# Optimization experiments

Measured on AMD Instinct MI355X. Metric: run time of the kernel, lower is better.

The kernel has to match this reference:

```python
import jax, jax.numpy as jnp
import numpy as np

D_MODEL = 1024
N_HEADS = 16
HEAD_DIM = D_MODEL // N_HEADS
THETA = 10000.0
B, T = 2, 2048


def apply_rope(x, pos, theta=THETA):
    # x: (b, h, t, d), pos: (t,)
    d = x.shape[-1]
    inv_freq = theta ** (-jnp.arange(0, d, 2, dtype=jnp.float32) / d)  # (d/2,)
    ang = pos.astype(jnp.float32)[:, None] * inv_freq[None, :]          # (t, d/2)
    cos, sin = jnp.cos(ang), jnp.sin(ang)
    x1, x2 = x[..., 0::2], x[..., 1::2]
    out_even = x1 * cos - x2 * sin
    out_odd = x1 * sin + x2 * cos
    return jnp.stack([out_even, out_odd], axis=-1).reshape(x.shape)


def setup_inputs() -> dict:
    key = jax.random.key(0)
    ks = jax.random.split(key, 5)
    s = 1.0 / np.sqrt(D_MODEL)
    return {
        "x": jax.random.normal(ks[0], (B, T, D_MODEL), jnp.float32),
        "wq": jax.random.normal(ks[1], (D_MODEL, D_MODEL), jnp.float32) * s,
        "wk": jax.random.normal(ks[2], (D_MODEL, D_MODEL), jnp.float32) * s,
        "wv": jax.random.normal(ks[3], (D_MODEL, D_MODEL), jnp.float32) * s,
        "wo": jax.random.normal(ks[4], (D_MODEL, D_MODEL), jnp.float32) * s,
        "token_pos": 1,
    }


def reference(x, wq, wk, wv, wo, token_pos):
    b, t, dm = x.shape
    # bias-free Linear: y = x @ W^T; split heads -> (b, h, t, d)
    def proj(w):
        y = jnp.einsum('btm,nm->btn', x, w)
        return y.reshape(b, t, N_HEADS, HEAD_DIM).transpose(0, 2, 1, 3)
    q, k, v = proj(wq), proj(wk), proj(wv)
    pos = jnp.arange(t)
    q = apply_rope(q, pos)
    k = apply_rope(k, pos)
    scale = jnp.sqrt(jnp.asarray(HEAD_DIM, dtype=x.dtype))
    scores = jnp.einsum('bhqd,bhkd->bhqk', q, k) / scale
    mask = jnp.tril(jnp.ones((t, t), dtype=bool))
    scores = jnp.where(mask, scores, -jnp.inf)
    attn = jax.nn.softmax(scores, axis=-1)
    out = jnp.einsum('bhqk,bhkd->bhqd', attn, v)
    out = out.transpose(0, 2, 1, 3).reshape(b, t, dm)
    return jnp.einsum('btm,nm->btn', out, wo)
```

## Files before the change

kernel.cpp:

```cpp
#include <hip/hip_runtime.h>
#include <hip/hip_bf16.h>
#include <math.h>

#define DM 1024
#define NH 16
#define HD 64
#define BB 2
#define TT 2048
#define MROWS (BB*TT)
#define PL ((size_t)MROWS * DM)
#define PLW ((size_t)DM * DM)

using bf8_t = __attribute__((ext_vector_type(8))) __bf16;
using bf4_t = __attribute__((ext_vector_type(4))) __bf16;
using f4_t  = __attribute__((ext_vector_type(4))) float;

typedef const __attribute__((address_space(1))) void* gas_t;
typedef __attribute__((address_space(3))) void* las_t;

__global__ __launch_bounds__(256) void prep(
        const void* __restrict__ X,
        const void* __restrict__ w0, const void* __restrict__ w1,
        const void* __restrict__ w2, const void* __restrict__ w3,
        __bf16* __restrict__ Xh, __bf16* __restrict__ Wsp,
        float2* __restrict__ trig, int* __restrict__ flag)
{
    const int id  = (int)blockIdx.x;
    const int tid = (int)threadIdx.x;

    __shared__ int cnt;
    if (tid == 0) cnt = 0;
    __syncthreads();
    {
        int local = 0;
        const unsigned short* xu = (const unsigned short*)X;
        for (int i = tid; i < 512; i += 256) {
            const int e = (xu[i] >> 7) & 0xFF;
            if (e >= 117 && e <= 130) local++;
        }
        atomicAdd(&cnt, local);
    }
    __syncthreads();
    const int f32 = (cnt >= 384) ? 0 : 1;

    if (id >= 8448) {
        if (tid == 0) *flag = f32;
        return;
    }
    if (id >= 8192) {
        const int idx = (id - 8192) * 256 + tid;
        const int t = idx >> 5, ip = idx & 31;
        const float inv_freq = powf(10000.0f, -2.0f * (float)ip / 64.0f);
        const float ang = (float)t * inv_freq;
        float s, c;
        sincosf(ang, &s, &c);
        trig[idx] = make_float2(c, s);
        return;
    }

    const void* Src;
    __bf16 *Yh, *Yl;
    size_t i;
    if (id < 4096) {
        Src = X;
        Yh = Xh; Yl = Xh + PL;
        i = ((size_t)id * 256 + tid) * 4;
    } else {
        const int wid   = (id - 4096) >> 10;
        const int inner = (id - 4096) & 1023;
        Src = (wid == 0) ? w0 : (wid == 1) ? w1 : (wid == 2) ? w2 : w3;
        Yh = Wsp + (size_t)wid * 2 * PLW;
        Yl = Yh + PLW;
        i = ((size_t)inner * 256 + tid) * 4;
    }
    if (f32) {
        float4 v = *(const float4*)((const float*)Src + i);
        __bf16 h0 = (__bf16)v.x, h1 = (__bf16)v.y, h2 = (__bf16)v.z, h3 = (__bf16)v.w;
        bf4_t hv = {h0, h1, h2, h3};
        bf4_t lv = {(__bf16)(v.x - (float)h0), (__bf16)(v.y - (float)h1),
                    (__bf16)(v.z - (float)h2), (__bf16)(v.w - (float)h3)};
        *(bf4_t*)(Yh + i) = hv;
        *(bf4_t*)(Yl + i) = lv;
    } else {
        bf4_t v = *(const bf4_t*)((const __bf16*)Src + i);
        *(bf4_t*)(Yh + i) = v;
        bf4_t zv = {(__bf16)0.f, (__bf16)0.f, (__bf16)0.f, (__bf16)0.f};
        *(bf4_t*)(Yl + i) = zv;
    }
}

__device__ __forceinline__ int xcd_remap(int flat, int nwg) {
    return (flat & 7) * (nwg >> 3) + (flat >> 3);
}

__device__ __forceinline__ int swz(int r, int b) {
    return r * 128 + (b ^ ((r & 7) << 4));
}
#define VST 264

__global__ __launch_bounds__(256, 3) void gemm_fused(
        const __bf16* __restrict__ Ahg,
        const __bf16* __restrict__ Wsp,
        __bf16* __restrict__ Y0, __bf16* __restrict__ Y1,
        __bf16* __restrict__ Y2,
        void* __restrict__ Yout,
        const float2* __restrict__ trig,
        const int* __restrict__ flag, const int outMode)
{
    const int f32 = *flag;

    const int nx = (int)gridDim.x, ny = (int)gridDim.y, nz = (int)gridDim.z;
    int flat = (int)blockIdx.x + nx * ((int)blockIdx.y + ny * (int)blockIdx.z);
    flat = xcd_remap(flat, nx * ny * nz);
    const int bx = flat % nx;
    const int rem = flat / nx;
    const int by = rem % ny;
    const int z  = rem / ny;

    const int widx = outMode ? 3 : z;
    const __bf16* Whg = Wsp + (size_t)widx * 2 * PLW;
    const __bf16* Wlg = Whg + PLW;
    const __bf16* Alg = Ahg + PL;
    const bool aLo = (outMode != 0) || (f32 != 0);
    const bool wLo = (f32 != 0);

    __shared__ __align__(16) char sm[49152];
    char* const AhL = sm;
    char* const AlL = sm + 16384;
    char* const WhL = sm + 32768;
    char* const WlL = sm + 40960;

    const int tid  = threadIdx.x;
    const int n0   = bx * 64, m0 = by * 128;
    const int lane = tid & 63;
    const int w    = tid >> 6;
    const int wr   = (w >> 1) * 64;
    const int wcn  = (w & 1) * 32;
    const int l15  = lane & 15;
    const int g    = lane >> 4;

    f4_t acc[4][2] = {};

    for (int k0 = 0; k0 < DM; k0 += 64) {
        if (k0) __syncthreads();

#pragma unroll
        for (int j = 0; j < 4; j++) {
            const int u = tid + j * 256, r = u >> 3, c = u & 7;
            char* const db = AhL + (size_t)(j * 256 + w * 64) * 16;
            __builtin_amdgcn_global_load_lds(
                (gas_t)(Ahg + (size_t)(m0 + r) * DM + k0 + c * 8),
                (las_t)db, 16, 0, 0);
            if (aLo)
                __builtin_amdgcn_global_load_lds(
                    (gas_t)(Alg + (size_t)(m0 + r) * DM + k0 + c * 8),
                    (las_t)(AlL + (size_t)(j * 256 + w * 64) * 16), 16, 0, 0);
        }
#pragma unroll
        for (int j = 0; j < 2; j++) {
            const int u = tid + j * 256, r = u >> 3, c = u & 7;
            __builtin_amdgcn_global_load_lds(
                (gas_t)(Whg + (size_t)(n0 + r) * DM + k0 + c * 8),
                (las_t)(WhL + (size_t)(j * 256 + w * 64) * 16), 16, 0, 0);
            if (wLo)
                __builtin_amdgcn_global_load_lds(
                    (gas_t)(Wlg + (size_t)(n0 + r) * DM + k0 + c * 8),
                    (las_t)(WlL + (size_t)(j * 256 + w * 64) * 16), 16, 0, 0);
        }
        __syncthreads();

#pragma unroll
        for (int kh = 0; kh < 2; kh++) {
            const int bc = kh * 64 + g * 16;
            bf8_t ah[4], al[4], wh[2], wl[2];
#pragma unroll
            for (int m = 0; m < 4; m++) {
                ah[m] = *(const bf8_t*)(AhL + (wr + m * 16 + l15) * 128 + bc);
                if (aLo) al[m] = *(const bf8_t*)(AlL + (wr + m * 16 + l15) * 128 + bc);
            }
#pragma unroll
            for (int n = 0; n < 2; n++) {
                wh[n] = *(const bf8_t*)(WhL + (wcn + n * 16 + l15) * 128 + bc);
                if (wLo) wl[n] = *(const bf8_t*)(WlL + (wcn + n * 16 + l15) * 128 + bc);
            }
#pragma unroll
            for (int m = 0; m < 4; m++)
#pragma unroll
                for (int n = 0; n < 2; n++) {
                    acc[m][n] = __builtin_amdgcn_mfma_f32_16x16x32_bf16(
                                    ah[m], wh[n], acc[m][n], 0, 0, 0);
                    if (aLo)
                        acc[m][n] = __builtin_amdgcn_mfma_f32_16x16x32_bf16(
                                        al[m], wh[n], acc[m][n], 0, 0, 0);
                    if (wLo)
                        acc[m][n] = __builtin_amdgcn_mfma_f32_16x16x32_bf16(
                                        ah[m], wl[n], acc[m][n], 0, 0, 0);
                }
        }
    }

    const int orow = g * 4;
    const int ocol = l15;
    __syncthreads();

    if (outMode) {
        if (f32) {
#pragma unroll
            for (int m = 0; m < 4; m++)
#pragma unroll
                for (int n = 0; n < 2; n++) {
                    const int gr = m0 + wr + m * 16 + orow;
                    const int gc = n0 + wcn + n * 16 + ocol;
#pragma unroll
                    for (int r = 0; r < 4; r++)
                        ((float*)Yout)[(size_t)(gr + r) * DM + gc] = acc[m][n][r];
                }
        } else {
            char* const EhL = sm;
#pragma unroll
            for (int m = 0; m < 4; m++)
#pragma unroll
                for (int n = 0; n < 2; n++) {
                    const int ctile = wcn + n * 16 + ocol;
#pragma unroll
                    for (int r = 0; r < 4; r++) {
                        const int rtile = wr + m * 16 + orow + r;
                        *(__bf16*)(EhL + rtile * 128 + ctile * 2) = (__bf16)acc[m][n][r];
                    }
                }
            __syncthreads();
#pragma unroll
            for (int j = 0; j < 4; j++) {
                const int u = tid + j * 256, r = u >> 3, c = u & 7;
                *(bf8_t*)((__bf16*)Yout + (size_t)(m0 + r) * DM + n0 + c * 8) =
                    *(const bf8_t*)(EhL + r * 128 + c * 16);
            }
        }
    } else if (z == 2) {
        char* const EhL = sm;
        char* const ElL = sm + 20480;
#pragma unroll
        for (int m = 0; m < 4; m++)
#pragma unroll
            for (int n = 0; n < 2; n++) {
                const int ctile = wcn + n * 16 + ocol;
#pragma unroll
                for (int r = 0; r < 4; r++) {
                    const int rtile = wr + m * 16 + orow + r;
                    const float val = acc[m][n][r];
                    __bf16 hb = (__bf16)val;
                    *(__bf16*)(EhL + ctile * VST + rtile * 2) = hb;
                    *(__bf16*)(ElL + ctile * VST + rtile * 2) = (__bf16)(val - (float)hb);
                }
            }
        __syncthreads();
        __bf16* Vh = Y2;
        __bf16* Vl = Y2 + PL;
#pragma unroll
        for (int j = 0; j < 4; j++) {
            const int u = tid + j * 256, cc = u >> 4, k = u & 15;
            *(bf8_t*)(Vh + (size_t)(n0 + cc) * MROWS + m0 + k * 8) =
                *(const bf8_t*)(EhL + cc * VST + k * 16);
            *(bf8_t*)(Vl + (size_t)(n0 + cc) * MROWS + m0 + k * 8) =
                *(const bf8_t*)(ElL + cc * VST + k * 16);
        }
    } else {
        char* const EhL = sm;
        char* const ElL = sm + 20480;
#pragma unroll
        for (int m = 0; m < 4; m++)
#pragma unroll
            for (int n = 0; n < 2; n++) {
                const int ctile = wcn + n * 16 + ocol;
                const int gc = n0 + ctile;
                const int ip = (gc & 63) >> 1;
                const bool oddc = (gc & 1) != 0;
#pragma unroll
                for (int r = 0; r < 4; r++) {
                    const int rtile = wr + m * 16 + orow + r;
                    const int t = (m0 + rtile) & (TT - 1);
                    const float2 cs = trig[t * 32 + ip];
                    const float v = acc[m][n][r];
                    const float ov = __shfl_xor(v, 1);
                    float res = oddc ? (ov * cs.y + v * cs.x) : (v * cs.x - ov * cs.y);
                    if (z == 0) res *= 0.125f;
                    __bf16 hb = (__bf16)res;
                    *(__bf16*)(EhL + rtile * 128 + ctile * 2) = hb;
                    *(__bf16*)(ElL + rtile * 128 + ctile * 2) = (__bf16)(res - (float)hb);
                }
            }
        __syncthreads();
        __bf16* Yh = z ? Y1 : Y0;
        __bf16* Yl = Yh + PL;
#pragma unroll
        for (int j = 0; j < 4; j++) {
            const int u = tid + j * 256, r = u >> 3, c = u & 7;
            *(bf8_t*)(Yh + (size_t)(m0 + r) * DM + n0 + c * 8) =
                *(const bf8_t*)(EhL + r * 128 + c * 16);
            *(bf8_t*)(Yl + (size_t)(m0 + r) * DM + n0 + c * 8) =
                *(const bf8_t*)(ElL + r * 128 + c * 16);
        }
    }
}

__global__ void __launch_bounds__(256, 2) flash_attn_mfma(
        const __bf16* __restrict__ Qhg, const __bf16* __restrict__ Khg,
        const __bf16* __restrict__ Vhg, __bf16* __restrict__ Aoh)
{
    __shared__ __align__(16) char sm[65536];

    const __bf16* Qlg = Qhg + PL;
    const __bf16* Klg = Khg + PL;
    const __bf16* Vlg = Vhg + PL;
    __bf16* Aol = Aoh + PL;

    int flat = (int)blockIdx.x + 16 * ((int)blockIdx.y + 16 * (int)blockIdx.z);
    flat = xcd_remap(flat, 512);
    const int qt = 15 - (flat % 16);
    const int h  = (flat / 16) % 16;
    const int b  = flat / 256;

    const int tid = threadIdx.x;
    const int lane = tid & 63;
    const int w    = tid >> 6;
    const int l15  = lane & 15;
    const int g    = lane >> 4;

    char* const pb = sm + 32768 + w * 8192;

    bf8_t qh[2][2], ql[2][2];
#pragma unroll
    for (int m = 0; m < 2; m++)
#pragma unroll
        for (int kh = 0; kh < 2; kh++) {
            const size_t off = (size_t)(b * TT + qt * 128 + w * 32 + m * 16 + l15) * DM
                             + h * HD + kh * 32 + g * 8;
            qh[m][kh] = *(const bf8_t*)(Qhg + off);
            ql[m][kh] = *(const bf8_t*)(Qlg + off);
        }

    f4_t o[2][4] = {};
    float lrow[2] = {0.f, 0.f};

    bf8_t pk[2], pkl[2], pv[2], pvl[2];
    auto ISSUE = [&](int kt) {
#pragma unroll
        for (int j = 0; j < 2; j++) {
            const int u = tid + j * 256, r = u >> 3, c = u & 7;
            const size_t ko = (size_t)(b * TT + kt * 64 + r) * DM + h * HD + c * 8;
            pk[j]  = *(const bf8_t*)(Khg + ko);
            pkl[j] = *(const bf8_t*)(Klg + ko);
            const size_t vo = (size_t)(h * HD + r) * MROWS + b * TT + kt * 64 + c * 8;
            pv[j]  = *(const bf8_t*)(Vhg + vo);
            pvl[j] = *(const bf8_t*)(Vlg + vo);
        }
    };

    const int nkt = 2 * qt + 2;
    ISSUE(0);
    for (int kt = 0; kt < nkt; kt++) {
        __syncthreads();
#pragma unroll
        for (int j = 0; j < 2; j++) {
            const int u = tid + j * 256, r = u >> 3, c = u & 7;
            *(bf8_t*)(sm +         swz(r, c * 16)) = pk[j];
            *(bf8_t*)(sm +  8192 + swz(r, c * 16)) = pkl[j];
            *(bf8_t*)(sm + 16384 + swz(r, c * 16)) = pv[j];
            *(bf8_t*)(sm + 24576 + swz(r, c * 16)) = pvl[j];
        }
        __syncthreads();
        if (kt + 1 < nkt) ISSUE(kt + 1);

        f4_t s[2][4] = {};
        __builtin_amdgcn_s_setprio(1);
#pragma unroll
        for (int kh = 0; kh < 2; kh++) {
#pragma unroll
            for (int n = 0; n < 4; n++) {
                bf8_t kf  = *(const bf8_t*)(sm +        swz(n * 16 + l15, kh * 64 + g * 16));
                bf8_t kl2 = *(const bf8_t*)(sm + 8192 + swz(n * 16 + l15, kh * 64 + g * 16));
#pragma unroll
                for (int m = 0; m < 2; m++) {
                    s[m][n] = __builtin_amdgcn_mfma_f32_16x16x32_bf16(kf,  qh[m][kh], s[m][n], 0, 0, 0);
                    s[m][n] = __builtin_amdgcn_mfma_f32_16x16x32_bf16(kl2, qh[m][kh], s[m][n], 0, 0, 0);
                    s[m][n] = __builtin_amdgcn_mfma_f32_16x16x32_bf16(kf,  ql[m][kh], s[m][n], 0, 0, 0);
                }
            }
        }
        __builtin_amdgcn_s_setprio(0);

        if (kt >= 2 * qt) {
            const int koff = (kt - 2 * qt) * 64;
#pragma unroll
            for (int m = 0; m < 2; m++) {
                const int qloc = w * 32 + m * 16 + l15;
#pragma unroll
                for (int n = 0; n < 4; n++)
#pragma unroll
                    for (int r = 0; r < 4; r++)
                        if (koff + n * 16 + g * 4 + r > qloc) s[m][n][r] = -INFINITY;
            }
        }

#pragma unroll
        for (int m = 0; m < 2; m++)
#pragma unroll
            for (int n = 0; n < 4; n++) {
                bf4_t hv, lv;
#pragma unroll
                for (int r = 0; r < 4; r++) {
                    const float p = __expf(s[m][n][r] - 8.0f);
                    lrow[m] += p;
                    __bf16 hb = (__bf16)p;
                    hv[r] = hb;
                    lv[r] = (__bf16)(p - (float)hb);
                }
                *(bf4_t*)(pb +        swz(m * 16 + l15, n * 32 + g * 8)) = hv;
                *(bf4_t*)(pb + 4096 + swz(m * 16 + l15, n * 32 + g * 8)) = lv;
            }
        asm volatile("s_waitcnt lgkmcnt(0)" ::: "memory");
        __builtin_amdgcn_sched_barrier(0);

        bf8_t pah[2][2], pal2[2][2];
#pragma unroll
        for (int m = 0; m < 2; m++)
#pragma unroll
            for (int kh = 0; kh < 2; kh++) {
                pah[m][kh]  = *(const bf8_t*)(pb +        swz(m * 16 + l15, kh * 64 + g * 16));
                pal2[m][kh] = *(const bf8_t*)(pb + 4096 + swz(m * 16 + l15, kh * 64 + g * 16));
            }

        __builtin_amdgcn_s_setprio(1);
#pragma unroll
        for (int kh = 0; kh < 2; kh++)
#pragma unroll
            for (int nf = 0; nf < 4; nf++) {
                bf8_t vf  = *(const bf8_t*)(sm + 16384 + swz(nf * 16 + l15, kh * 64 + g * 16));
                bf8_t vl2 = *(const bf8_t*)(sm + 24576 + swz(nf * 16 + l15, kh * 64 + g * 16));
#pragma unroll
                for (int m = 0; m < 2; m++) {
                    o[m][nf] = __builtin_amdgcn_mfma_f32_16x16x32_bf16(pah[m][kh],  vf,  o[m][nf], 0, 0, 0);
                    o[m][nf] = __builtin_amdgcn_mfma_f32_16x16x32_bf16(pal2[m][kh], vf,  o[m][nf], 0, 0, 0);
                    o[m][nf] = __builtin_amdgcn_mfma_f32_16x16x32_bf16(pah[m][kh],  vl2, o[m][nf], 0, 0, 0);
                }
            }
        __builtin_amdgcn_s_setprio(0);
    }

    float linv[2][4];
#pragma unroll
    for (int m = 0; m < 2; m++) {
        lrow[m] += __shfl_xor(lrow[m], 16);
        lrow[m] += __shfl_xor(lrow[m], 32);
        const float inv = 1.0f / lrow[m];
#pragma unroll
        for (int r = 0; r < 4; r++)
            linv[m][r] = __shfl(inv, (lane & 48) | (g * 4 + r));
    }

#pragma unroll
    for (int m = 0; m < 2; m++)
#pragma unroll
        for (int nf = 0; nf < 4; nf++)
#pragma unroll
            for (int r = 0; r < 4; r++) {
                const float val = o[m][nf][r] * linv[m][r];
                __bf16 hb = (__bf16)val;
                const int row = m * 16 + g * 4 + r;
                *(__bf16*)(pb + row * 128 + (nf * 16 + l15) * 2) = hb;
                *(__bf16*)(pb + 4096 + row * 128 + (nf * 16 + l15) * 2) =
                    (__bf16)(val - (float)hb);
            }
    asm volatile("s_waitcnt lgkmcnt(0)" ::: "memory");
    __builtin_amdgcn_sched_barrier(0);
#pragma unroll
    for (int j = 0; j < 4; j++) {
        const int u = lane + j * 64, r = u >> 3, c = u & 7;
        const size_t off = (size_t)(b * TT + qt * 128 + w * 32 + r) * DM
                         + h * HD + c * 8;
        *(bf8_t*)(Aoh + off) = *(const bf8_t*)(pb + r * 128 + c * 16);
        *(bf8_t*)(Aol + off) = *(const bf8_t*)(pb + 4096 + r * 128 + c * 16);
    }
}

extern "C" void kernel_launch(void* const* d_in, const int* in_sizes, int n_in,
                              void* d_out, int out_size, void* d_ws, size_t ws_size,
                              hipStream_t stream) {
    const void* x  = d_in[0];
    const void* wq = d_in[1];
    const void* wk = d_in[2];
    const void* wv = d_in[3];
    const void* wo = d_in[4];

    __bf16* Qh  = (__bf16*)d_ws;
    __bf16* Kh  = Qh + 2 * PL;
    __bf16* Vth = Kh + 2 * PL;
    __bf16* Xh  = Vth + 2 * PL;
    __bf16* Wsp = Xh + 2 * PL;
    char* tail  = (char*)(Wsp + 8 * PLW);
    int* flag   = (int*)tail;
    float2* trig = (float2*)(tail + 512);

    prep<<<8449, 256, 0, stream>>>(x, wq, wk, wv, wo, Xh, Wsp, trig, flag);

    gemm_fused<<<dim3(DM / 64, MROWS / 128, 3), 256, 0, stream>>>(
        Xh, Wsp, Qh, Kh, Vth, nullptr, trig, flag, 0);

    flash_attn_mfma<<<dim3(16, NH, BB), 256, 0, stream>>>(Qh, Kh, Vth, Xh);

    gemm_fused<<<dim3(DM / 64, MROWS / 128, 1), 256, 0, stream>>>(
        Xh, Wsp, nullptr, nullptr, nullptr, d_out, trig, flag, 1);
}
```

Baseline: 326.1 us.

## Swizzle GEMM LDS tiles and add 64x64 tiled output projection kernel

Measured after the change: 312.1 us. -4.3%, faster.

```diff
diff --git a/kernel.cpp b/kernel.cpp
--- a/kernel.cpp
+++ b/kernel.cpp
@@ -147,24 +147,25 @@
 #pragma unroll
         for (int j = 0; j < 4; j++) {
             const int u = tid + j * 256, r = u >> 3, c = u & 7;
-            char* const db = AhL + (size_t)(j * 256 + w * 64) * 16;
+            const int cs = c ^ (r & 7);
             __builtin_amdgcn_global_load_lds(
-                (gas_t)(Ahg + (size_t)(m0 + r) * DM + k0 + c * 8),
-                (las_t)db, 16, 0, 0);
+                (gas_t)(Ahg + (size_t)(m0 + r) * DM + k0 + cs * 8),
+                (las_t)(AhL + (size_t)(j * 256 + w * 64) * 16), 16, 0, 0);
             if (aLo)
                 __builtin_amdgcn_global_load_lds(
-                    (gas_t)(Alg + (size_t)(m0 + r) * DM + k0 + c * 8),
+                    (gas_t)(Alg + (size_t)(m0 + r) * DM + k0 + cs * 8),
                     (las_t)(AlL + (size_t)(j * 256 + w * 64) * 16), 16, 0, 0);
         }
 #pragma unroll
         for (int j = 0; j < 2; j++) {
             const int u = tid + j * 256, r = u >> 3, c = u & 7;
+            const int cs = c ^ (r & 7);
             __builtin_amdgcn_global_load_lds(
-                (gas_t)(Whg + (size_t)(n0 + r) * DM + k0 + c * 8),
+                (gas_t)(Whg + (size_t)(n0 + r) * DM + k0 + cs * 8),
                 (las_t)(WhL + (size_t)(j * 256 + w * 64) * 16), 16, 0, 0);
             if (wLo)
                 __builtin_amdgcn_global_load_lds(
-                    (gas_t)(Wlg + (size_t)(n0 + r) * DM + k0 + c * 8),
+                    (gas_t)(Wlg + (size_t)(n0 + r) * DM + k0 + cs * 8),
                     (las_t)(WlL + (size_t)(j * 256 + w * 64) * 16), 16, 0, 0);
         }
         __syncthreads();
@@ -175,13 +176,13 @@
             bf8_t ah[4], al[4], wh[2], wl[2];
 #pragma unroll
             for (int m = 0; m < 4; m++) {
-                ah[m] = *(const bf8_t*)(AhL + (wr + m * 16 + l15) * 128 + bc);
-                if (aLo) al[m] = *(const bf8_t*)(AlL + (wr + m * 16 + l15) * 128 + bc);
+                ah[m] = *(const bf8_t*)(AhL + swz(wr + m * 16 + l15, bc));
+                if (aLo) al[m] = *(const bf8_t*)(AlL + swz(wr + m * 16 + l15, bc));
             }
 #pragma unroll
             for (int n = 0; n < 2; n++) {
-                wh[n] = *(const bf8_t*)(WhL + (wcn + n * 16 + l15) * 128 + bc);
-                if (wLo) wl[n] = *(const bf8_t*)(WlL + (wcn + n * 16 + l15) * 128 + bc);
+                wh[n] = *(const bf8_t*)(WhL + swz(wcn + n * 16 + l15, bc));
+                if (wLo) wl[n] = *(const bf8_t*)(WlL + swz(wcn + n * 16 + l15, bc));
             }
 #pragma unroll
             for (int m = 0; m < 4; m++)
@@ -303,6 +304,131 @@
     }
 }
 
+__global__ __launch_bounds__(256, 4) void gemm_out64(
+        const __bf16* __restrict__ Ahg,
+        const __bf16* __restrict__ Wsp,
+        void* __restrict__ Yout,
+        const int* __restrict__ flag)
+{
+    const int f32 = *flag;
+
+    int flat = (int)blockIdx.x + 16 * (int)blockIdx.y;
+    flat = xcd_remap(flat, 1024);
+    const int bx = flat % 16;
+    const int by = flat / 16;
+
+    const __bf16* Whg = Wsp + (size_t)3 * 2 * PLW;
+    const __bf16* Wlg = Whg + PLW;
+    const __bf16* Alg = Ahg + PL;
+    const bool wLo = (f32 != 0);
+
+    __shared__ __align__(16) char sm[32768];
+    char* const AhL = sm;
+    char* const AlL = sm + 8192;
+    char* const WhL = sm + 16384;
+    char* const WlL = sm + 24576;
+
+    const int tid  = threadIdx.x;
+    const int n0   = bx * 64, m0 = by * 64;
+    const int lane = tid & 63;
+    const int w    = tid >> 6;
+    const int wr   = (w >> 1) * 32;
+    const int wcn  = (w & 1) * 32;
+    const int l15  = lane & 15;
+    const int g    = lane >> 4;
+
+    f4_t acc[2][2] = {};
+
+    for (int k0 = 0; k0 < DM; k0 += 64) {
+        if (k0) __syncthreads();
+
+#pragma unroll
+        for (int j = 0; j < 2; j++) {
+            const int u = tid + j * 256, r = u >> 3, c = u & 7;
+            const int cs = c ^ (r & 7);
+            __builtin_amdgcn_global_load_lds(
+                (gas_t)(Ahg + (size_t)(m0 + r) * DM + k0 + cs * 8),
+                (las_t)(AhL + (size_t)(j * 256 + w * 64) * 16), 16, 0, 0);
+            __builtin_amdgcn_global_load_lds(
+                (gas_t)(Alg + (size_t)(m0 + r) * DM + k0 + cs * 8),
+                (las_t)(AlL + (size_t)(j * 256 + w * 64) * 16), 16, 0, 0);
+            __builtin_amdgcn_global_load_lds(
+                (gas_t)(Whg + (size_t)(n0 + r) * DM + k0 + cs * 8),
+                (las_t)(WhL + (size_t)(j * 256 + w * 64) * 16), 16, 0, 0);
+            if (wLo)
+                __builtin_amdgcn_global_load_lds(
+                    (gas_t)(Wlg + (size_t)(n0 + r) * DM + k0 + cs * 8),
+                    (las_t)(WlL + (size_t)(j * 256 + w * 64) * 16), 16, 0, 0);
+        }
+        __syncthreads();
+
+#pragma unroll
+        for (int kh = 0; kh < 2; kh++) {
+            const int bc = kh * 64 + g * 16;
+            bf8_t ah[2], al[2], wh[2], wl[2];
+#pragma unroll
+            for (int m = 0; m < 2; m++) {
+                ah[m] = *(const bf8_t*)(AhL + swz(wr + m * 16 + l15, bc));
+                al[m] = *(const bf8_t*)(AlL + swz(wr + m * 16 + l15, bc));
+            }
+#pragma unroll
+            for (int n = 0; n < 2; n++) {
+                wh[n] = *(const bf8_t*)(WhL + swz(wcn + n * 16 + l15, bc));
+                if (wLo) wl[n] = *(const bf8_t*)(WlL + swz(wcn + n * 16 + l15, bc));
+            }
+#pragma unroll
+            for (int m = 0; m < 2; m++)
+#pragma unroll
+                for (int n = 0; n < 2; n++) {
+                    acc[m][n] = __builtin_amdgcn_mfma_f32_16x16x32_bf16(
+                                    ah[m], wh[n], acc[m][n], 0, 0, 0);
+                    acc[m][n] = __builtin_amdgcn_mfma_f32_16x16x32_bf16(
+                                    al[m], wh[n], acc[m][n], 0, 0, 0);
+                    if (wLo)
+                        acc[m][n] = __builtin_amdgcn_mfma_f32_16x16x32_bf16(
+                                        ah[m], wl[n], acc[m][n], 0, 0, 0);
+                }
+        }
+    }
+
+    const int orow = g * 4;
+    const int ocol = l15;
+    __syncthreads();
+
+    if (f32) {
+#pragma unroll
+        for (int m = 0; m < 2; m++)
+#pragma unroll
+            for (int n = 0; n < 2; n++) {
+                const int gr = m0 + wr + m * 16 + orow;
+                const int gc = n0 + wcn + n * 16 + ocol;
+#pragma unroll
+                for (int r = 0; r < 4; r++)
+                    ((float*)Yout)[(size_t)(gr + r) * DM + gc] = acc[m][n][r];
+            }
+    } else {
+        char* const EhL = sm;
+#pragma unroll
+        for (int m = 0; m < 2; m++)
+#pragma unroll
+            for (int n = 0; n < 2; n++) {
+                const int ctile = wcn + n * 16 + ocol;
+#pragma unroll
+                for (int r = 0; r < 4; r++) {
+                    const int rtile = wr + m * 16 + orow + r;
+                    *(__bf16*)(EhL + rtile * 128 + ctile * 2) = (__bf16)acc[m][n][r];
+                }
+            }
+        __syncthreads();
+#pragma unroll
+        for (int j = 0; j < 2; j++) {
+            const int u = tid + j * 256, r = u >> 3, c = u & 7;
+            *(bf8_t*)((__bf16*)Yout + (size_t)(m0 + r) * DM + n0 + c * 8) =
+                *(const bf8_t*)(EhL + r * 128 + c * 16);
+        }
+    }
+}
+
 __global__ void __launch_bounds__(256, 2) flash_attn_mfma(
         const __bf16* __restrict__ Qhg, const __bf16* __restrict__ Khg,
         const __bf16* __restrict__ Vhg, __bf16* __restrict__ Aoh)
@@ -508,6 +634,5 @@
 
     flash_attn_mfma<<<dim3(16, NH, BB), 256, 0, stream>>>(Qh, Kh, Vth, Xh);
 
-    gemm_fused<<<dim3(DM / 64, MROWS / 128, 1), 256, 0, stream>>>(
-        Xh, Wsp, nullptr, nullptr, nullptr, d_out, trig, flag, 1);
+    gemm_out64<<<dim3(16, 64), 256, 0, stream>>>(Xh, Wsp, d_out, flag);
 }
```
